# Performance work log

Measured on AMD Instinct MI355X. Metric: run time of the kernel, lower is better.

Reference implementation:

```python
import jax, jax.numpy as jnp
import numpy as np

HIDDEN = 1024
INNER = 2048  # hidden * expand_factor
STATE = 64
K = 4  # conv kernel size
BATCH, SEQ = 2, 2048


def setup_inputs() -> dict:
    key = jax.random.key(0)
    ks = jax.random.split(key, 8)
    def w(k, shape, scale=0.02):
        return (jax.random.normal(k, shape, jnp.float32) * scale)
    return {
        "x": jax.random.normal(ks[0], (BATCH, SEQ, HIDDEN), jnp.float32),
        "W_in": w(ks[1], (HIDDEN, 2 * INNER)),
        "conv_w": w(ks[2], (INNER, 1, K), 0.2),   # depthwise conv kernel [O, I/groups=1, K]
        "conv_b": jnp.zeros((INNER,), jnp.float32),
        "W_dt": w(ks[3], (INNER, INNER)),
        "b_dt": jnp.linspace(-4.0, -2.0, INNER).astype(jnp.float32),  # log(exp(linspace)) = linspace
        "W_B": w(ks[4], (INNER, STATE)),
        "W_C": w(ks[5], (INNER, STATE)),
        "D": jnp.ones((INNER,), jnp.float32),
        "W_out": w(ks[6], (INNER, HIDDEN)),
    }


def reference(x, W_in, conv_w, conv_b, W_dt, b_dt, W_B, W_C, D, W_out):
    batch, seq_len, _ = x.shape
    inner = W_dt.shape[0]
    state_dim = W_B.shape[1]

    # input projection and gate split
    xz = x @ W_in                              # [B, L, 2*inner]
    x_inner, z = jnp.split(xz, 2, axis=-1)

    # causal depthwise conv1d (pad both sides by K-1 then truncate == left-pad K-1)
    xc = jnp.transpose(x_inner, (0, 2, 1))    # [B, inner, L]
    k = conv_w.shape[-1]
    xc = jax.lax.conv_general_dilated(
        xc, conv_w, window_strides=(1,), padding=[(k - 1, 0)],
        dimension_numbers=("NCH", "OIH", "NCH"), feature_group_count=inner)
    xc = xc + conv_b[None, :, None]
    xc = jax.nn.silu(jnp.transpose(xc, (0, 2, 1)))   # [B, L, inner]

    # selective SSM parameters
    dt = jax.nn.softplus(xc @ W_dt + b_dt)    # [B, L, inner]
    Bm = xc @ W_B                             # [B, L, N]
    Cm = xc @ W_C                             # [B, L, N]
    a = jnp.exp(-dt)                          # [B, L, inner]
    dtx = dt * xc                             # [B, L, inner]

    # sequential selective scan over time: state[B, inner, N]
    def step(state, inp):
        a_t, dtx_t, b_t, c_t = inp
        state = a_t[..., None] * state + dtx_t[..., None] * b_t[:, None, :]
        y_t = jnp.einsum("bin,bn->bi", state, c_t)
        return state, y_t

    init = jnp.zeros((batch, inner, state_dim), x.dtype)
    xs = (jnp.swapaxes(a, 0, 1), jnp.swapaxes(dtx, 0, 1),
          jnp.swapaxes(Bm, 0, 1), jnp.swapaxes(Cm, 0, 1))
    _, ys = jax.lax.scan(step, init, xs)      # ys: [L, B, inner]
    y = jnp.swapaxes(ys, 0, 1) + D * xc       # skip connection

    y = y * jax.nn.silu(z)                    # output gate
    return y @ W_out                          # [B, L, hidden]
```

## Files before the change

### kernel.cpp

```cpp
#include <hip/hip_runtime.h>
#include <hip/hip_bf16.h>
#include <math.h>

#define BATCH  2
#define SEQ    2048
#define HID    1024
#define INNER  2048
#define NSTATE 64
#define NTOK   (BATCH * SEQ)
#define TCHUNK 64
#define NCHUNK (SEQ / TCHUNK)
#define NMID   (INNER + 2 * NSTATE)
#define LDH    1056
#define LDI    2080

typedef __bf16 bf16x8 __attribute__((ext_vector_type(8)));
typedef float  f32x4  __attribute__((ext_vector_type(4)));

typedef const __attribute__((address_space(1))) char* gas_ptr;
typedef __attribute__((address_space(3))) char*       las_ptr;

__device__ __forceinline__ void gload16(const void* g, void* l) {
  __builtin_amdgcn_global_load_lds((gas_ptr)g, (las_ptr)l, 16, 0, 0);
}

__device__ __forceinline__ unsigned short f2bf(float f) {
  __hip_bfloat16 h = __float2bfloat16(f);
  return __builtin_bit_cast(unsigned short, h);
}
__device__ __forceinline__ float bf2f(unsigned short u) {
  unsigned int x = ((unsigned int)u) << 16;
  return __builtin_bit_cast(float, x);
}

__global__ __launch_bounds__(256) void cvt_pad_kernel(
    const float* __restrict__ in, __hip_bfloat16* __restrict__ out, int n4) {
  int i = blockIdx.x * 256 + threadIdx.x;
  if (i >= n4) return;
  const int r = i >> 8;
  const int c = (i & 255) * 4;
  float4 v = *(const float4*)&in[(size_t)r * HID + c];
  ushort4 u;
  u.x = f2bf(v.x); u.y = f2bf(v.y); u.z = f2bf(v.z); u.w = f2bf(v.w);
  *(ushort4*)&out[(size_t)r * LDH + c] = u;
}

__global__ __launch_bounds__(256) void transpose_cvt_kernel(
    const float* __restrict__ in, __hip_bfloat16* __restrict__ out,
    int R, int C, int ostride) {
  __shared__ float tile[32][33];
  int tx = threadIdx.x & 31, ty = threadIdx.x >> 5;
  int c0 = blockIdx.x * 32, r0 = blockIdx.y * 32;
#pragma unroll
  for (int i = 0; i < 4; ++i)
    tile[ty + 8 * i][tx] = in[(size_t)(r0 + ty + 8 * i) * C + c0 + tx];
  __syncthreads();
#pragma unroll
  for (int i = 0; i < 4; ++i)
    out[(size_t)(c0 + ty + 8 * i) * ostride + r0 + tx] =
        __float2bfloat16(tile[tx][ty + 8 * i]);
}

template <int EPI>
__global__ __launch_bounds__(256, 4) void gemm_bt_kernel(
    const __hip_bfloat16* __restrict__ A, const __hip_bfloat16* __restrict__ Bt,
    int M, int N, int Klen, int ldk, int gridN, int nwg, int mnwg,
    float* __restrict__ Cout, int ldc, int ldo,
    __hip_bfloat16* __restrict__ o0, __hip_bfloat16* __restrict__ o1) {
  __shared__ __align__(16) __hip_bfloat16 As[128 * 64];
  __shared__ __align__(16) __hip_bfloat16 Bs[128 * 64];
  const int tid = threadIdx.x;
  const int lane = tid & 63;
  const int w = tid >> 6;
  const int wr = w >> 1, wc = w & 1;

  const int orig = blockIdx.x;
  const int q8 = nwg >> 3, r8 = nwg & 7;
  const int xcd = orig & 7, seq = orig >> 3;
  const int wg = (xcd < r8 ? xcd * (q8 + 1) : r8 * (q8 + 1) + (xcd - r8) * q8) + seq;
  const int kz = wg / mnwg;
  const int wgr = wg - kz * mnwg;
  const int m0 = (wgr / gridN) * 128;
  const int n0 = (wgr % gridN) * 128;

  const __hip_bfloat16* Ab = A + (size_t)kz * Klen;
  const __hip_bfloat16* Bb = Bt + (size_t)kz * Klen;

  f32x4 acc[4][4];
#pragma unroll
  for (int i = 0; i < 4; ++i)
#pragma unroll
    for (int j = 0; j < 4; ++j)
#pragma unroll
      for (int r2 = 0; r2 < 4; ++r2) acc[i][j][r2] = 0.f;

  const int g8row = lane >> 3;
  const int scol = ((lane & 7) ^ g8row) * 8;
  const __hip_bfloat16* Agp = Ab + (size_t)(m0 + w * 32 + g8row) * ldk + scol;
  const __hip_bfloat16* Bgp = Bb + (size_t)(n0 + w * 32 + g8row) * ldk + scol;
  __hip_bfloat16* lA = As + (w * 32) * 64;
  __hip_bfloat16* lB = Bs + (w * 32) * 64;

  const int lrow = lane & 15, lk = lane >> 4;
  const int arow0 = wr * 64 + lrow;
  const int brow0 = wc * 64 + lrow;

  const int nt = Klen >> 6;
  for (int t = 0; t < nt; ++t) {
    __syncthreads();
#pragma unroll
    for (int g = 0; g < 4; ++g) {
      gload16(Agp + (size_t)(g * 8) * ldk + t * 64, lA + (g * 8) * 64);
      gload16(Bgp + (size_t)(g * 8) * ldk + t * 64, lB + (g * 8) * 64);
    }
    __syncthreads();
#pragma unroll
    for (int ss = 0; ss < 2; ++ss) {
      bf16x8 af[4], bv[4];
#pragma unroll
      for (int i = 0; i < 4; ++i) {
        const int ra = arow0 + i * 16;
        af[i] = *(const bf16x8*)(As + ra * 64 + (((ss * 4 + lk) ^ (ra & 7)) * 8));
        const int rb = brow0 + i * 16;
        bv[i] = *(const bf16x8*)(Bs + rb * 64 + (((ss * 4 + lk) ^ (rb & 7)) * 8));
      }
#pragma unroll
      for (int i = 0; i < 4; ++i)
#pragma unroll
        for (int j = 0; j < 4; ++j)
          acc[i][j] = __builtin_amdgcn_mfma_f32_16x16x32_bf16(af[i], bv[j], acc[i][j], 0, 0, 0);
    }
  }

#pragma unroll
  for (int i = 0; i < 4; ++i) {
#pragma unroll
    for (int j = 0; j < 4; ++j) {
#pragma unroll
      for (int r2 = 0; r2 < 4; ++r2) {
        const int row = m0 + wr * 64 + i * 16 + lk * 4 + r2;
        const int col = n0 + wc * 64 + j * 16 + lrow;
        const float v = acc[i][j][r2];
        if constexpr (EPI == 0) {
          Cout[(size_t)kz * M * ldc + (size_t)row * ldc + col] = v;
        } else {
          if (col < INNER) o0[(size_t)row * ldo + col] = __float2bfloat16(v);
          else             o1[(size_t)row * ldo + (col - INNER)] = __float2bfloat16(v);
        }
      }
    }
  }
}

__global__ __launch_bounds__(256) void reduce_mid_kernel(
    const float* __restrict__ P, const float* __restrict__ bdt,
    const __hip_bfloat16* __restrict__ xch, unsigned int* __restrict__ dtx,
    float* __restrict__ Bm, float* __restrict__ Cm) {
  const int i = blockIdx.x * 256 + threadIdx.x;
  const int row = i / (NMID / 4);
  const int c4 = i - row * (NMID / 4);
  const int col = c4 * 4;
  const size_t off = (size_t)row * NMID + col;
  float4 a = *(const float4*)&P[off];
  float4 b = *(const float4*)&P[(size_t)NTOK * NMID + off];
  float4 v = make_float4(a.x + b.x, a.y + b.y, a.z + b.z, a.w + b.w);
  if (col < INNER) {
    float4 bb = *(const float4*)&bdt[col];
    float4 d;
    d.x = v.x + bb.x; d.y = v.y + bb.y; d.z = v.z + bb.z; d.w = v.w + bb.w;
    d.x = (d.x > 15.f) ? d.x : log1pf(__expf(d.x));
    d.y = (d.y > 15.f) ? d.y : log1pf(__expf(d.y));
    d.z = (d.z > 15.f) ? d.z : log1pf(__expf(d.z));
    d.w = (d.w > 15.f) ? d.w : log1pf(__expf(d.w));
    ushort4 xv = *(const ushort4*)&xch[(size_t)row * LDI + col];
    uint4 o;
    o.x = (unsigned int)f2bf(d.x) | ((unsigned int)xv.x << 16);
    o.y = (unsigned int)f2bf(d.y) | ((unsigned int)xv.y << 16);
    o.z = (unsigned int)f2bf(d.z) | ((unsigned int)xv.z << 16);
    o.w = (unsigned int)f2bf(d.w) | ((unsigned int)xv.w << 16);
    *(uint4*)&dtx[(size_t)row * LDI + col] = o;
  } else if (col < INNER + NSTATE) {
    *(float4*)&Bm[(size_t)row * NSTATE + (col - INNER)] = v;
  } else {
    *(float4*)&Cm[(size_t)row * NSTATE + (col - INNER - NSTATE)] = v;
  }
}

__global__ __launch_bounds__(256) void reduce4_kernel(
    const float* __restrict__ P, float* __restrict__ out, int n4) {
  int i = blockIdx.x * 256 + threadIdx.x;
  if (i >= n4) return;
  float4 a = ((const float4*)P)[i];
  float4 b = ((const float4*)P)[i + n4];
  float4 c = ((const float4*)P)[i + 2 * n4];
  float4 d = ((const float4*)P)[i + 3 * n4];
  ((float4*)out)[i] = make_float4((a.x + b.x) + (c.x + d.x), (a.y + b.y) + (c.y + d.y),
                                  (a.z + b.z) + (c.z + d.z), (a.w + b.w) + (c.w + d.w));
}

__global__ __launch_bounds__(256) void conv_silu_kernel(
    const __hip_bfloat16* __restrict__ xin, const float* __restrict__ cw,
    const float* __restrict__ cb, __hip_bfloat16* __restrict__ xch) {
  int idx = blockIdx.x * 256 + threadIdx.x;
  int cg = idx & 511;
  int tok = idx >> 9;
  int c = cg * 4;
  int l = tok & (SEQ - 1);
  float wv[4][4];
#pragma unroll
  for (int i = 0; i < 4; ++i) {
    float4 w = *(const float4*)&cw[(c + i) * 4];
    wv[i][0] = w.x; wv[i][1] = w.y; wv[i][2] = w.z; wv[i][3] = w.w;
  }
  float4 bias = *(const float4*)&cb[c];
  float r0 = bias.x, r1 = bias.y, r2 = bias.z, r3 = bias.w;
#pragma unroll
  for (int k = 0; k < 4; ++k) {
    const int d = 3 - k;
    if (l >= d) {
      ushort4 xv = *(const ushort4*)&xin[(size_t)(tok - d) * LDI + c];
      r0 = fmaf(bf2f(xv.x), wv[0][k], r0);
      r1 = fmaf(bf2f(xv.y), wv[1][k], r1);
      r2 = fmaf(bf2f(xv.z), wv[2][k], r2);
      r3 = fmaf(bf2f(xv.w), wv[3][k], r3);
    }
  }
  r0 = r0 / (1.f + __expf(-r0));
  r1 = r1 / (1.f + __expf(-r1));
  r2 = r2 / (1.f + __expf(-r2));
  r3 = r3 / (1.f + __expf(-r3));
  ushort4 u;
  u.x = f2bf(r0); u.y = f2bf(r1); u.z = f2bf(r2); u.w = f2bf(r3);
  *(ushort4*)&xch[(size_t)tok * LDI + c] = u;
}

__global__ __launch_bounds__(256) void cumv_kernel(
    const unsigned int* __restrict__ dtx, float* __restrict__ cumA,
    unsigned int* __restrict__ wT) {
  const int bk = blockIdx.y;
  const int c = blockIdx.x * 256 + threadIdx.x;
  const int b = bk >> 5, k = bk & 31;
  const size_t tokbase = (size_t)(b * SEQ + k * TCHUNK);
  float cum = 1.f;
  unsigned int wreg[32];
#pragma unroll
  for (int t = 0; t < TCHUNK; ++t) {
    const unsigned int pk = dtx[(tokbase + t) * LDI + c];
    const float dtv = bf2f((unsigned short)(pk & 0xffffu));
    const float xc = bf2f((unsigned short)(pk >> 16));
    cum *= __expf(-dtv);
    cum = fmaxf(cum, 1e-30f);
    cumA[(tokbase + t) * INNER + c] = cum;
    const unsigned short wb = f2bf(dtv * xc / cum);
    if (t & 1) wreg[t >> 1] |= ((unsigned int)wb) << 16;
    else       wreg[t >> 1] = (unsigned int)wb;
  }
  uint4* dst = (uint4*)(wT + ((size_t)bk * INNER + c) * 32);
#pragma unroll
  for (int j = 0; j < 8; ++j)
    dst[j] = make_uint4(wreg[4 * j], wreg[4 * j + 1], wreg[4 * j + 2], wreg[4 * j + 3]);
}

__global__ __launch_bounds__(256) void chunkG_kernel(
    const float* __restrict__ Bm, const float* __restrict__ Cm,
    __hip_bfloat16* __restrict__ Abuf, __hip_bfloat16* __restrict__ BtBuf) {
  __shared__ float Bsh[TCHUNK][NSTATE + 4];
  __shared__ float Csh[TCHUNK][NSTATE + 4];
  const int bk = blockIdx.x;
  const int b = bk >> 5, k = bk & 31;
  const int tid = threadIdx.x;
  const size_t tokbase = (size_t)(b * SEQ + k * TCHUNK);
  for (int i = tid; i < TCHUNK * 16; i += 256) {
    const int row = i >> 4, q = i & 15;
    *(float4*)&Bsh[row][q * 4] = *(const float4*)&Bm[(tokbase + row) * NSTATE + q * 4];
    *(float4*)&Csh[row][q * 4] = *(const float4*)&Cm[(tokbase + row) * NSTATE + q * 4];
  }
  __syncthreads();
  for (int e = tid; e < 64 * 64; e += 256) {
    const int t = e >> 6, tau = e & 63;
    float g = 0.f;
    if (tau <= t) {
#pragma unroll
      for (int q = 0; q < 16; ++q) {
        const float4 cv = *(const float4*)&Csh[t][q * 4];
        const float4 bv = *(const float4*)&Bsh[tau][q * 4];
        g += cv.x * bv.x + cv.y * bv.y + cv.z * bv.z + cv.w * bv.w;
      }
    }
    Abuf[((size_t)bk * 64 + t) * 128 + tau] = __float2bfloat16(g);
  }
  for (int e = tid; e < 64 * 64; e += 256) {
    const int n2 = e >> 6, r = e & 63;
    BtBuf[((size_t)bk * 64 + n2) * 64 + r] = __float2bfloat16(Bsh[r][n2]);
    Abuf[((size_t)bk * 64 + n2) * 128 + 64 + r] = __float2bfloat16(Csh[n2][r]);
  }
}

__global__ __launch_bounds__(256, 4) void sloc_gemm_kernel(
    const __hip_bfloat16* __restrict__ wT, const __hip_bfloat16* __restrict__ BtBuf,
    const float* __restrict__ cumA, float* __restrict__ S) {
  __shared__ __align__(16) __hip_bfloat16 As[128 * 64];
  __shared__ __align__(16) __hip_bfloat16 Bs[64 * 64];
  const int tid = threadIdx.x;
  const int lane = tid & 63;
  const int w = tid >> 6;
  const int bk = blockIdx.x >> 4;
  const int ct = blockIdx.x & 15;
  const int b = bk >> 5, k = bk & 31;
  const int c0 = ct * 128;

  const int g8row = lane >> 3;
  const int scol = ((lane & 7) ^ g8row) * 8;
  const __hip_bfloat16* Ag = wT + ((size_t)bk * INNER + c0 + w * 32 + g8row) * 64 + scol;
  const __hip_bfloat16* Bg = BtBuf + ((size_t)bk * 64 + w * 16 + g8row) * 64 + scol;
  __hip_bfloat16* lA = As + (w * 32) * 64;
  __hip_bfloat16* lB = Bs + (w * 16) * 64;
#pragma unroll
  for (int g = 0; g < 4; ++g) gload16(Ag + (size_t)(g * 8) * 64, lA + (g * 8) * 64);
#pragma unroll
  for (int g = 0; g < 2; ++g) gload16(Bg + (size_t)(g * 8) * 64, lB + (g * 8) * 64);
  __syncthreads();

  const int lrow = lane & 15, lk = lane >> 4;
  f32x4 acc[2][4];
#pragma unroll
  for (int i = 0; i < 2; ++i)
#pragma unroll
    for (int j = 0; j < 4; ++j)
#pragma unroll
      for (int r2 = 0; r2 < 4; ++r2) acc[i][j][r2] = 0.f;

#pragma unroll
  for (int ss = 0; ss < 2; ++ss) {
    bf16x8 af[2], bv[4];
#pragma unroll
    for (int i = 0; i < 2; ++i) {
      const int ra = w * 32 + i * 16 + lrow;
      af[i] = *(const bf16x8*)(As + ra * 64 + (((ss * 4 + lk) ^ (ra & 7)) * 8));
    }
#pragma unroll
    for (int j = 0; j < 4; ++j) {
      const int rb = j * 16 + lrow;
      bv[j] = *(const bf16x8*)(Bs + rb * 64 + (((ss * 4 + lk) ^ (rb & 7)) * 8));
    }
#pragma unroll
    for (int i = 0; i < 2; ++i)
#pragma unroll
      for (int j = 0; j < 4; ++j)
        acc[i][j] = __builtin_amdgcn_mfma_f32_16x16x32_bf16(af[i], bv[j], acc[i][j], 0, 0, 0);
  }

  const size_t tokT = (size_t)(b * SEQ + k * TCHUNK + 63);
#pragma unroll
  for (int i = 0; i < 2; ++i) {
#pragma unroll
    for (int j = 0; j < 4; ++j) {
#pragma unroll
      for (int r2 = 0; r2 < 4; ++r2) {
        const int c = c0 + w * 32 + i * 16 + lk * 4 + r2;
        const int n = j * 16 + lrow;
        const float sc = cumA[tokT * INNER + c];
        S[((size_t)bk * INNER + c) * 64 + n] = acc[i][j][r2] * sc;
      }
    }
  }
}

__global__ __launch_bounds__(256) void scan_combine_kernel(
    float* __restrict__ S, const float* __restrict__ cumA) {
  const int idx = blockIdx.x * 256 + threadIdx.x;
  const int n = idx & 63;
  const int c = (idx >> 6) & (INNER - 1);
  const int b = idx >> 17;
  float s = 0.f;
  for (int k = 0; k < NCHUNK; ++k) {
    const size_t cs = (size_t)(b * NCHUNK + k) * INNER + c;
    const size_t off = cs * 64 + n;
    const float loc = S[off];
    S[off] = s;
    const float ak = cumA[((size_t)(b * SEQ + k * TCHUNK + 63)) * INNER + c];
    s = fmaf(ak, s, loc);
  }
}

__global__ __launch_bounds__(256, 4) void ypre_gemm_kernel(
    const __hip_bfloat16* __restrict__ Abuf, const __hip_bfloat16* __restrict__ wT,
    const float* __restrict__ S, const float* __restrict__ cumA,
    const __hip_bfloat16* __restrict__ xch, const __hip_bfloat16* __restrict__ zbf,
    const float* __restrict__ Dv, __hip_bfloat16* __restrict__ ygated) {
  __shared__ __align__(16) __hip_bfloat16 Asm[64 * 128];
  __shared__ __align__(16) __hip_bfloat16 Bsm[128 * 128];
  const int tid = threadIdx.x;
  const int lane = tid & 63;
  const int w = tid >> 6;
  const int bk = blockIdx.x >> 4;
  const int ct = blockIdx.x & 15;
  const int b = bk >> 5, k = bk & 31;
  const int c0 = ct * 128;

  {
#pragma unroll
    for (int g = 0; g < 4; ++g) {
      const int base = w * 16 + g * 4;
      const int col16s = (lane & 15) ^ ((base + (lane >> 4)) & 7);
      const __hip_bfloat16* src =
          Abuf + ((size_t)bk * 64 + base + (lane >> 4)) * 128 + col16s * 8;
      gload16(src, (char*)Asm + base * 256);
    }
  }
  {
    const int row = tid & 127, part = tid >> 7;
    const int c = c0 + row;
    if (part == 0) {
      const uint4* src = (const uint4*)(wT + ((size_t)bk * INNER + c) * 64);
#pragma unroll
      for (int s2 = 0; s2 < 8; ++s2) {
        uint4 v = src[s2];
        *(uint4*)((char*)Bsm + row * 256 + (s2 ^ (row & 7)) * 16) = v;
      }
    } else {
      const float* srcS = S + ((size_t)bk * INNER + c) * 64;
#pragma unroll
      for (int s2 = 0; s2 < 8; ++s2) {
        float4 a2 = *(const float4*)&srcS[s2 * 8];
        float4 b2 = *(const float4*)&srcS[s2 * 8 + 4];
        uint4 v;
        v.x = (unsigned)f2bf(a2.x) | ((unsigned)f2bf(a2.y) << 16);
        v.y = (unsigned)f2bf(a2.z) | ((unsigned)f2bf(a2.w) << 16);
        v.z = (unsigned)f2bf(b2.x) | ((unsigned)f2bf(b2.y) << 16);
        v.w = (unsigned)f2bf(b2.z) | ((unsigned)f2bf(b2.w) << 16);
        *(uint4*)((char*)Bsm + row * 256 + ((8 + s2) ^ (row & 7)) * 16) = v;
      }
    }
  }
  __syncthreads();

  const int lrow = lane & 15, lk = lane >> 4;
  f32x4 acc[8];
#pragma unroll
  for (int j = 0; j < 8; ++j)
#pragma unroll
    for (int r2 = 0; r2 < 4; ++r2) acc[j][r2] = 0.f;

  const int ra = w * 16 + lrow;
#pragma unroll
  for (int kk = 0; kk < 4; ++kk) {
    const int csa = (kk * 4 + lk) ^ (ra & 7);
    bf16x8 af = *(const bf16x8*)((const char*)Asm + ra * 256 + csa * 16);
#pragma unroll
    for (int j = 0; j < 8; ++j) {
      const int rb = j * 16 + lrow;
      const int csb = (kk * 4 + lk) ^ (rb & 7);
      bf16x8 bv = *(const bf16x8*)((const char*)Bsm + rb * 256 + csb * 16);
      acc[j] = __builtin_amdgcn_mfma_f32_16x16x32_bf16(af, bv, acc[j], 0, 0, 0);
    }
  }

  const size_t tokb = (size_t)(b * SEQ + k * TCHUNK);
#pragma unroll
  for (int j = 0; j < 8; ++j) {
#pragma unroll
    for (int r2 = 0; r2 < 4; ++r2) {
      const int t = w * 16 + lk * 4 + r2;
      const int c = c0 + j * 16 + lrow;
      const size_t tok = tokb + t;
      const float ca = cumA[tok * INNER + c];
      const float xc = bf2f(*(const unsigned short*)&xch[tok * LDI + c]);
      const float z = bf2f(*(const unsigned short*)&zbf[tok * LDI + c]);
      const float yt = ca * acc[j][r2] + Dv[c] * xc;
      const float g = z / (1.f + __expf(-z));
      *(unsigned short*)&ygated[tok * LDI + c] = f2bf(yt * g);
    }
  }
}

extern "C" void kernel_launch(void* const* d_in, const int* in_sizes, int n_in,
                              void* d_out, int out_size, void* d_ws, size_t ws_size,
                              hipStream_t stream) {
  const float* x      = (const float*)d_in[0];
  const float* W_in   = (const float*)d_in[1];
  const float* conv_w = (const float*)d_in[2];
  const float* conv_b = (const float*)d_in[3];
  const float* W_dt   = (const float*)d_in[4];
  const float* b_dt   = (const float*)d_in[5];
  const float* W_B    = (const float*)d_in[6];
  const float* W_C    = (const float*)d_in[7];
  const float* Dvec   = (const float*)d_in[8];
  const float* W_out  = (const float*)d_in[9];
  float* out = (float*)d_out;

  char* p = (char*)d_ws;
  auto alloc = [&](size_t bytes) {
    char* r = p;
    p += (bytes + 255) & ~(size_t)255;
    return r;
  };
  __hip_bfloat16* xin   = (__hip_bfloat16*)alloc((size_t)NTOK * LDI * 2);
  __hip_bfloat16* zbf   = (__hip_bfloat16*)alloc((size_t)NTOK * LDI * 2);
  char*           scr   = alloc((size_t)NTOK * LDH * 2 + (size_t)2 * INNER * LDH * 2);
  __hip_bfloat16* WmidT = (__hip_bfloat16*)alloc((size_t)NMID * LDI * 2);
  __hip_bfloat16* WoutT = (__hip_bfloat16*)alloc((size_t)HID * LDI * 2);
  unsigned int*   dtx   = (unsigned int*)alloc((size_t)NTOK * LDI * 4);
  float*          Bm    = (float*)alloc((size_t)NTOK * NSTATE * 4);
  float*          Cm    = (float*)alloc((size_t)NTOK * NSTATE * 4);
  float*          cumA  = (float*)alloc((size_t)NTOK * INNER * 4);
  __hip_bfloat16* wT    = (__hip_bfloat16*)alloc((size_t)BATCH * NCHUNK * INNER * TCHUNK * 2);
  __hip_bfloat16* Abuf  = (__hip_bfloat16*)alloc((size_t)BATCH * NCHUNK * 64 * 128 * 2);
  __hip_bfloat16* BtBuf = (__hip_bfloat16*)alloc((size_t)BATCH * NCHUNK * 64 * 64 * 2);
  float*          Pmid  = (float*)alloc((size_t)2 * NTOK * NMID * 4);

  __hip_bfloat16* x_bf   = (__hip_bfloat16*)scr;
  __hip_bfloat16* WinT   = (__hip_bfloat16*)(scr + (size_t)NTOK * LDH * 2);
  __hip_bfloat16* xch    = (__hip_bfloat16*)scr;
  __hip_bfloat16* ygated = xin;
  float*          S      = Pmid;
  float*          Pout   = Pmid;

  cvt_pad_kernel<<<(NTOK * HID / 4 + 255) / 256, 256, 0, stream>>>(x, x_bf, NTOK * HID / 4);
  transpose_cvt_kernel<<<dim3((2 * INNER) / 32, HID / 32), 256, 0, stream>>>(W_in, WinT, HID, 2 * INNER, LDH);
  transpose_cvt_kernel<<<dim3(INNER / 32, INNER / 32), 256, 0, stream>>>(W_dt, WmidT, INNER, INNER, LDI);
  transpose_cvt_kernel<<<dim3(NSTATE / 32, INNER / 32), 256, 0, stream>>>(
      W_B, WmidT + (size_t)INNER * LDI, INNER, NSTATE, LDI);
  transpose_cvt_kernel<<<dim3(NSTATE / 32, INNER / 32), 256, 0, stream>>>(
      W_C, WmidT + (size_t)(INNER + NSTATE) * LDI, INNER, NSTATE, LDI);
  transpose_cvt_kernel<<<dim3(HID / 32, INNER / 32), 256, 0, stream>>>(W_out, WoutT, INNER, HID, LDI);

  {
    const int gridN = (2 * INNER) / 128, nwg = (NTOK / 128) * gridN;
    gemm_bt_kernel<1><<<nwg, 256, 0, stream>>>(
        x_bf, WinT, NTOK, 2 * INNER, HID, LDH, gridN, nwg, nwg, nullptr, 0, LDI, xin, zbf);
  }

  conv_silu_kernel<<<(NTOK * (INNER / 4)) / 256, 256, 0, stream>>>(xin, conv_w, conv_b, xch);

  {
    const int gridN = NMID / 128;
    const int mnwg = (NTOK / 128) * gridN;
    const int nwg = mnwg * 2;
    gemm_bt_kernel<0><<<nwg, 256, 0, stream>>>(
        xch, WmidT, NTOK, NMID, INNER / 2, LDI, gridN, nwg, mnwg, Pmid, NMID, 0,
        nullptr, nullptr);
    reduce_mid_kernel<<<(NTOK * (NMID / 4)) / 256, 256, 0, stream>>>(Pmid, b_dt, xch, dtx, Bm, Cm);
  }

  cumv_kernel<<<dim3(INNER / 256, BATCH * NCHUNK), 256, 0, stream>>>(dtx, cumA, (unsigned int*)wT);
  chunkG_kernel<<<BATCH * NCHUNK, 256, 0, stream>>>(Bm, Cm, Abuf, BtBuf);
  sloc_gemm_kernel<<<BATCH * NCHUNK * 16, 256, 0, stream>>>(wT, BtBuf, cumA, S);
  scan_combine_kernel<<<(BATCH * INNER * NSTATE) / 256, 256, 0, stream>>>(S, cumA);
  ypre_gemm_kernel<<<BATCH * NCHUNK * 16, 256, 0, stream>>>(
      Abuf, wT, S, cumA, xch, zbf, Dvec, ygated);

  {
    const int gridN = HID / 128;
    const int mnwg = (NTOK / 128) * gridN;
    const int nwg = mnwg * 4;
    gemm_bt_kernel<0><<<nwg, 256, 0, stream>>>(
        ygated, WoutT, NTOK, HID, INNER / 4, LDI, gridN, nwg, mnwg, Pout, HID, 0,
        nullptr, nullptr);
    const int n4 = NTOK * HID / 4;
    reduce4_kernel<<<(n4 + 255) / 256, 256, 0, stream>>>(Pout, out, n4);
  }
}
```

Baseline: 327.7 us.

## Store split-K partials, scan states and cumulative decay in bf16

Adds a GEMM epilogue that writes split-K partial sums as bf16 instead of fp32, and switches the reduce kernels to read bf16 partials. The cumulative decay array cumA and the chunk state tensor S also move from fp32 to bf16 across the cumv, sloc, scan-combine and ypre kernels. The aim is to halve global memory traffic for these intermediates, at the cost of precision loss in partial sums, decay products (which can be very small) and the recurrent state carried across chunks.

New measurement: 308.6 us. 1.06x faster.

```diff
diff --git a/kernel.cpp b/kernel.cpp
--- a/kernel.cpp
+++ b/kernel.cpp
@@ -143,9 +143,11 @@
         const float v = acc[i][j][r2];
         if constexpr (EPI == 0) {
           Cout[(size_t)kz * M * ldc + (size_t)row * ldc + col] = v;
-        } else {
+        } else if constexpr (EPI == 1) {
           if (col < INNER) o0[(size_t)row * ldo + col] = __float2bfloat16(v);
           else             o1[(size_t)row * ldo + (col - INNER)] = __float2bfloat16(v);
+        } else {
+          o0[(size_t)kz * M * ldc + (size_t)row * ldc + col] = __float2bfloat16(v);
         }
       }
     }
@@ -153,17 +155,19 @@
 }
 
 __global__ __launch_bounds__(256) void reduce_mid_kernel(
-    const float* __restrict__ P, const float* __restrict__ bdt,
+    const __hip_bfloat16* __restrict__ P, const float* __restrict__ bdt,
     const __hip_bfloat16* __restrict__ xch, unsigned int* __restrict__ dtx,
     float* __restrict__ Bm, float* __restrict__ Cm) {
   const int i = blockIdx.x * 256 + threadIdx.x;
   const int row = i / (NMID / 4);
   const int c4 = i - row * (NMID / 4);
   const int col = c4 * 4;
-  const size_t off = (size_t)row * NMID + col;
-  float4 a = *(const float4*)&P[off];
-  float4 b = *(const float4*)&P[(size_t)NTOK * NMID + off];
-  float4 v = make_float4(a.x + b.x, a.y + b.y, a.z + b.z, a.w + b.w);
+  float4 v = make_float4(0.f, 0.f, 0.f, 0.f);
+#pragma unroll
+  for (int pp = 0; pp < 2; ++pp) {
+    const ushort4 u = *(const ushort4*)&P[(size_t)pp * NTOK * NMID + (size_t)row * NMID + col];
+    v.x += bf2f(u.x); v.y += bf2f(u.y); v.z += bf2f(u.z); v.w += bf2f(u.w);
+  }
   if (col < INNER) {
     float4 bb = *(const float4*)&bdt[col];
     float4 d;
@@ -186,16 +190,17 @@
   }
 }
 
-__global__ __launch_bounds__(256) void reduce4_kernel(
-    const float* __restrict__ P, float* __restrict__ out, int n4) {
+__global__ __launch_bounds__(256) void reduce4b_kernel(
+    const __hip_bfloat16* __restrict__ P, float* __restrict__ out, int n4) {
   int i = blockIdx.x * 256 + threadIdx.x;
   if (i >= n4) return;
-  float4 a = ((const float4*)P)[i];
-  float4 b = ((const float4*)P)[i + n4];
-  float4 c = ((const float4*)P)[i + 2 * n4];
-  float4 d = ((const float4*)P)[i + 3 * n4];
-  ((float4*)out)[i] = make_float4((a.x + b.x) + (c.x + d.x), (a.y + b.y) + (c.y + d.y),
-                                  (a.z + b.z) + (c.z + d.z), (a.w + b.w) + (c.w + d.w));
+  float4 acc = make_float4(0.f, 0.f, 0.f, 0.f);
+#pragma unroll
+  for (int pp = 0; pp < 4; ++pp) {
+    ushort4 u = ((const ushort4*)P)[(size_t)pp * n4 + i];
+    acc.x += bf2f(u.x); acc.y += bf2f(u.y); acc.z += bf2f(u.z); acc.w += bf2f(u.w);
+  }
+  ((float4*)out)[i] = acc;
 }
 
 __global__ __launch_bounds__(256) void conv_silu_kernel(
@@ -235,7 +240,7 @@
 }
 
 __global__ __launch_bounds__(256) void cumv_kernel(
-    const unsigned int* __restrict__ dtx, float* __restrict__ cumA,
+    const unsigned int* __restrict__ dtx, unsigned short* __restrict__ cumA,
     unsigned int* __restrict__ wT) {
   const int bk = blockIdx.y;
   const int c = blockIdx.x * 256 + threadIdx.x;
@@ -250,7 +255,7 @@
     const float xc = bf2f((unsigned short)(pk >> 16));
     cum *= __expf(-dtv);
     cum = fmaxf(cum, 1e-30f);
-    cumA[(tokbase + t) * INNER + c] = cum;
+    cumA[(tokbase + t) * INNER + c] = f2bf(cum);
     const unsigned short wb = f2bf(dtv * xc / cum);
     if (t & 1) wreg[t >> 1] |= ((unsigned int)wb) << 16;
     else       wreg[t >> 1] = (unsigned int)wb;
@@ -298,7 +303,7 @@
 
 __global__ __launch_bounds__(256, 4) void sloc_gemm_kernel(
     const __hip_bfloat16* __restrict__ wT, const __hip_bfloat16* __restrict__ BtBuf,
-    const float* __restrict__ cumA, float* __restrict__ S) {
+    const unsigned short* __restrict__ cumA, unsigned short* __restrict__ S) {
   __shared__ __align__(16) __hip_bfloat16 As[128 * 64];
   __shared__ __align__(16) __hip_bfloat16 Bs[64 * 64];
   const int tid = threadIdx.x;
@@ -359,15 +364,15 @@
       for (int r2 = 0; r2 < 4; ++r2) {
         const int c = c0 + w * 32 + i * 16 + lk * 4 + r2;
         const int n = j * 16 + lrow;
-        const float sc = cumA[tokT * INNER + c];
-        S[((size_t)bk * INNER + c) * 64 + n] = acc[i][j][r2] * sc;
+        const float sc = bf2f(cumA[tokT * INNER + c]);
+        S[((size_t)bk * INNER + c) * 64 + n] = f2bf(acc[i][j][r2] * sc);
       }
     }
   }
 }
 
 __global__ __launch_bounds__(256) void scan_combine_kernel(
-    float* __restrict__ S, const float* __restrict__ cumA) {
+    unsigned short* __restrict__ S, const unsigned short* __restrict__ cumA) {
   const int idx = blockIdx.x * 256 + threadIdx.x;
   const int n = idx & 63;
   const int c = (idx >> 6) & (INNER - 1);
@@ -376,16 +381,16 @@
   for (int k = 0; k < NCHUNK; ++k) {
     const size_t cs = (size_t)(b * NCHUNK + k) * INNER + c;
     const size_t off = cs * 64 + n;
-    const float loc = S[off];
-    S[off] = s;
-    const float ak = cumA[((size_t)(b * SEQ + k * TCHUNK + 63)) * INNER + c];
+    const float loc = bf2f(S[off]);
+    S[off] = f2bf(s);
+    const float ak = bf2f(cumA[((size_t)(b * SEQ + k * TCHUNK + 63)) * INNER + c]);
     s = fmaf(ak, s, loc);
   }
 }
 
 __global__ __launch_bounds__(256, 4) void ypre_gemm_kernel(
     const __hip_bfloat16* __restrict__ Abuf, const __hip_bfloat16* __restrict__ wT,
-    const float* __restrict__ S, const float* __restrict__ cumA,
+    const unsigned short* __restrict__ S, const unsigned short* __restrict__ cumA,
     const __hip_bfloat16* __restrict__ xch, const __hip_bfloat16* __restrict__ zbf,
     const float* __restrict__ Dv, __hip_bfloat16* __restrict__ ygated) {
   __shared__ __align__(16) __hip_bfloat16 Asm[64 * 128];
@@ -419,16 +424,10 @@
         *(uint4*)((char*)Bsm + row * 256 + (s2 ^ (row & 7)) * 16) = v;
       }
     } else {
-      const float* srcS = S + ((size_t)bk * INNER + c) * 64;
+      const uint4* srcS = (const uint4*)(S + ((size_t)bk * INNER + c) * 64);
 #pragma unroll
       for (int s2 = 0; s2 < 8; ++s2) {
-        float4 a2 = *(const float4*)&srcS[s2 * 8];
-        float4 b2 = *(const float4*)&srcS[s2 * 8 + 4];
-        uint4 v;
-        v.x = (unsigned)f2bf(a2.x) | ((unsigned)f2bf(a2.y) << 16);
-        v.y = (unsigned)f2bf(a2.z) | ((unsigned)f2bf(a2.w) << 16);
-        v.z = (unsigned)f2bf(b2.x) | ((unsigned)f2bf(b2.y) << 16);
-        v.w = (unsigned)f2bf(b2.z) | ((unsigned)f2bf(b2.w) << 16);
+        uint4 v = srcS[s2];
         *(uint4*)((char*)Bsm + row * 256 + ((8 + s2) ^ (row & 7)) * 16) = v;
       }
     }
@@ -464,7 +463,7 @@
       const int t = w * 16 + lk * 4 + r2;
       const int c = c0 + j * 16 + lrow;
       const size_t tok = tokb + t;
-      const float ca = cumA[tok * INNER + c];
+      const float ca = bf2f(cumA[tok * INNER + c]);
       const float xc = bf2f(*(const unsigned short*)&xch[tok * LDI + c]);
       const float z = bf2f(*(const unsigned short*)&zbf[tok * LDI + c]);
       const float yt = ca * acc[j][r2] + Dv[c] * xc;
@@ -503,18 +502,18 @@
   unsigned int*   dtx   = (unsigned int*)alloc((size_t)NTOK * LDI * 4);
   float*          Bm    = (float*)alloc((size_t)NTOK * NSTATE * 4);
   float*          Cm    = (float*)alloc((size_t)NTOK * NSTATE * 4);
-  float*          cumA  = (float*)alloc((size_t)NTOK * INNER * 4);
+  unsigned short* cumA  = (unsigned short*)alloc((size_t)NTOK * INNER * 2);
   __hip_bfloat16* wT    = (__hip_bfloat16*)alloc((size_t)BATCH * NCHUNK * INNER * TCHUNK * 2);
   __hip_bfloat16* Abuf  = (__hip_bfloat16*)alloc((size_t)BATCH * NCHUNK * 64 * 128 * 2);
   __hip_bfloat16* BtBuf = (__hip_bfloat16*)alloc((size_t)BATCH * NCHUNK * 64 * 64 * 2);
-  float*          Pmid  = (float*)alloc((size_t)2 * NTOK * NMID * 4);
+  __hip_bfloat16* Pmid  = (__hip_bfloat16*)alloc((size_t)2 * NTOK * NMID * 2);
 
   __hip_bfloat16* x_bf   = (__hip_bfloat16*)scr;
   __hip_bfloat16* WinT   = (__hip_bfloat16*)(scr + (size_t)NTOK * LDH * 2);
   __hip_bfloat16* xch    = (__hip_bfloat16*)scr;
   __hip_bfloat16* ygated = xin;
-  float*          S      = Pmid;
-  float*          Pout   = Pmid;
+  unsigned short* S      = (unsigned short*)Pmid;
+  __hip_bfloat16* Pout   = Pmid;
 
   cvt_pad_kernel<<<(NTOK * HID / 4 + 255) / 256, 256, 0, stream>>>(x, x_bf, NTOK * HID / 4);
   transpose_cvt_kernel<<<dim3((2 * INNER) / 32, HID / 32), 256, 0, stream>>>(W_in, WinT, HID, 2 * INNER, LDH);
@@ -537,9 +536,9 @@
     const int gridN = NMID / 128;
     const int mnwg = (NTOK / 128) * gridN;
     const int nwg = mnwg * 2;
-    gemm_bt_kernel<0><<<nwg, 256, 0, stream>>>(
-        xch, WmidT, NTOK, NMID, INNER / 2, LDI, gridN, nwg, mnwg, Pmid, NMID, 0,
-        nullptr, nullptr);
+    gemm_bt_kernel<2><<<nwg, 256, 0, stream>>>(
+        xch, WmidT, NTOK, NMID, INNER / 2, LDI, gridN, nwg, mnwg, nullptr, NMID, 0,
+        Pmid, nullptr);
     reduce_mid_kernel<<<(NTOK * (NMID / 4)) / 256, 256, 0, stream>>>(Pmid, b_dt, xch, dtx, Bm, Cm);
   }
 
@@ -554,10 +553,10 @@
     const int gridN = HID / 128;
     const int mnwg = (NTOK / 128) * gridN;
     const int nwg = mnwg * 4;
-    gemm_bt_kernel<0><<<nwg, 256, 0, stream>>>(
-        ygated, WoutT, NTOK, HID, INNER / 4, LDI, gridN, nwg, mnwg, Pout, HID, 0,
-        nullptr, nullptr);
+    gemm_bt_kernel<2><<<nwg, 256, 0, stream>>>(
+        ygated, WoutT, NTOK, HID, INNER / 4, LDI, gridN, nwg, mnwg, nullptr, HID, 0,
+        Pout, nullptr);
     const int n4 = NTOK * HID / 4;
-    reduce4_kernel<<<(n4 + 255) / 256, 256, 0, stream>>>(Pout, out, n4);
-  }
-}
+    reduce4b_kernel<<<(n4 + 255) / 256, 256, 0, stream>>>(Pout, out, n4);
+  }
+}
```
